# Optimization experiments

Measured on AMD Instinct MI355X. Metric: run time of the kernel, lower is better.

Reference implementation:

```python
import jax, jax.numpy as jnp
import numpy as np

N_NODES = 50000
N_EDGES = 800000
IN_DIM = 128
HID = 64
N_LAYERS = 4  # num_layers=5 in source -> 4 GINConv layers
BN_EPS = 1e-5


def setup_inputs() -> dict:
    key = jax.random.key(0)
    ks = jax.random.split(key, 16)
    h = jax.random.normal(ks[0], (N_NODES, IN_DIM), dtype=jnp.float32)
    src = jax.random.randint(ks[1], (N_EDGES,), 0, N_NODES, dtype=jnp.int32)
    dst = jax.random.randint(ks[2], (N_EDGES,), 0, N_NODES, dtype=jnp.int32)
    s = 0.05
    # layer 0 params (IN_DIM -> HID -> HID)
    W1_0 = jax.random.normal(ks[3], (IN_DIM, HID), dtype=jnp.float32) * s
    b1_0 = jnp.zeros((HID,), jnp.float32)
    W2_0 = jax.random.normal(ks[4], (HID, HID), dtype=jnp.float32) * s
    b2_0 = jnp.zeros((HID,), jnp.float32)
    g_0 = jnp.ones((HID,), jnp.float32)
    be_0 = jnp.zeros((HID,), jnp.float32)
    # layers 1..3 params stacked (HID -> HID -> HID)
    W1s = jax.random.normal(ks[5], (N_LAYERS - 1, HID, HID), dtype=jnp.float32) * s
    b1s = jnp.zeros((N_LAYERS - 1, HID), jnp.float32)
    W2s = jax.random.normal(ks[6], (N_LAYERS - 1, HID, HID), dtype=jnp.float32) * s
    b2s = jnp.zeros((N_LAYERS - 1, HID), jnp.float32)
    gs = jnp.ones((N_LAYERS - 1, HID), jnp.float32)
    bes = jnp.zeros((N_LAYERS - 1, HID), jnp.float32)
    return dict(h=h, src=src, dst=dst,
                W1_0=W1_0, b1_0=b1_0, W2_0=W2_0, b2_0=b2_0, g_0=g_0, be_0=be_0,
                W1s=W1s, b1s=b1s, W2s=W2s, b2s=b2s, gs=gs, bes=bes)


def _gin_layer(h, src, dst, W1, b1, W2, b2, gamma, beta):
    # GINConv (eps=0, sum aggregation): z = h + sum_{j->i} h_j
    agg = jax.ops.segment_sum(h[src], dst, num_segments=N_NODES)  # [N, d]
    z = h + agg
    # MLP: Linear -> ReLU -> Linear
    z = jax.nn.relu(z @ W1 + b1) @ W2 + b2
    # BatchNorm1d (training mode: batch statistics over nodes)
    mean = jnp.mean(z, axis=0)
    var = jnp.var(z, axis=0)
    z = (z - mean) * jax.lax.rsqrt(var + BN_EPS) * gamma + beta
    return jax.nn.relu(z)


def reference(h, src, dst, W1_0, b1_0, W2_0, b2_0, g_0, be_0,
              W1s, b1s, W2s, b2s, gs, bes):
    h = _gin_layer(h, src, dst, W1_0, b1_0, W2_0, b2_0, g_0, be_0)
    for i in range(N_LAYERS - 1):
        h = _gin_layer(h, src, dst, W1s[i], b1s[i], W2s[i], b2s[i], gs[i], bes[i])
    return h
```

## Files before the change

kernel.cpp:

```cpp
#include <hip/hip_runtime.h>
#include <hip/hip_bf16.h>

static constexpr int NN = 50000;
static constexpr int NE = 800000;
static constexpr float BN_EPS = 1e-5f;

static constexpr int NB  = 128;
static constexpr int NPB = 391;
static constexpr int CAP = 8192;
static constexpr int CHUNK = 2048;
static constexpr int SRNG = 12500;

static constexpr int BINABLK  = (NE + CHUNK - 1) / CHUNK;
static constexpr int PROJ0BLK = (NN + 63) / 64;

typedef short bf16x8 __attribute__((ext_vector_type(8)));
typedef float f32x4 __attribute__((ext_vector_type(4)));

__device__ __forceinline__ float bflo(unsigned u) { return __uint_as_float(u << 16); }
__device__ __forceinline__ float bfhi(unsigned u) { return __uint_as_float(u & 0xffff0000u); }
__device__ __forceinline__ unsigned short f2bf(float f) {
    unsigned u = __float_as_uint(f);
    unsigned r = (u + 0x7fffu + ((u >> 16) & 1u)) >> 16;
    return (unsigned short)r;
}

__global__ __launch_bounds__(256) void zero_kernel(int* __restrict__ ptr, int n)
{
    int i = blockIdx.x * 256 + threadIdx.x;
    if (i < n) ptr[i] = 0;
}

struct SmBinA {
    unsigned stage[CHUNK];
    int hist[NB], base[NB], gpos[NB];
};
struct SmProj0 {
    unsigned short Wt[64][136];
};

__device__ __forceinline__ void binA_body(
    SmBinA& sm, const int* __restrict__ src, const int* __restrict__ dst,
    int* __restrict__ gcount, unsigned* __restrict__ tmp, int blk)
{
    const int t = threadIdx.x;
    const int cb = blk * CHUNK;
    const int total = min(CHUNK, NE - cb);

    if (t < NB) sm.hist[t] = 0;
    __syncthreads();

    int mb[8], mslot[8];
    unsigned mv[8];
    #pragma unroll
    for (int k = 0; k < 8; ++k) {
        int e = cb + k * 256 + t;
        mb[k] = -1;
        if (e < NE) {
            int s = src[e];
            int d = dst[e];
            int b = d / NPB;
            mb[k] = b;
            mv[k] = ((unsigned)d << 16) | (unsigned)s;
            mslot[k] = atomicAdd(&sm.hist[b], 1);
        }
    }
    __syncthreads();

    if (t < NB) sm.base[t] = sm.hist[t];
    __syncthreads();
    for (int ofs = 1; ofs < NB; ofs <<= 1) {
        int v = (t >= ofs && t < NB) ? sm.base[t - ofs] : 0;
        __syncthreads();
        if (t < NB) sm.base[t] += v;
        __syncthreads();
    }
    if (t < NB && sm.hist[t] > 0)
        sm.gpos[t] = t * CAP + atomicAdd(&gcount[t], sm.hist[t]);
    __syncthreads();

    #pragma unroll
    for (int k = 0; k < 8; ++k) {
        if (mb[k] >= 0) {
            int b = mb[k];
            sm.stage[(sm.base[b] - sm.hist[b]) + mslot[k]] = mv[k];
        }
    }
    __syncthreads();

    for (int i = t; i < total; i += 256) {
        unsigned v = sm.stage[i];
        int b = (int)(v >> 16) / NPB;
        int pos = sm.gpos[b] + (i - (sm.base[b] - sm.hist[b]));
        tmp[pos] = v;
    }
}

__device__ __forceinline__ void proj0_body(
    SmProj0& sm, const float* __restrict__ hin, const float* __restrict__ W1,
    unsigned short* __restrict__ p, int blk)
{
    const int t = threadIdx.x;
    for (int i = t; i < 128 * 16; i += 256) {
        int k = i >> 4, c0 = (i & 15) * 4;
        float4 w = *reinterpret_cast<const float4*>(W1 + (size_t)k * 64 + c0);
        sm.Wt[c0 + 0][k] = f2bf(w.x); sm.Wt[c0 + 1][k] = f2bf(w.y);
        sm.Wt[c0 + 2][k] = f2bf(w.z); sm.Wt[c0 + 3][k] = f2bf(w.w);
    }
    __syncthreads();

    const int wv = t >> 6;
    const int l = t & 63;
    const int g = l >> 4;
    const int cl = l & 15;
    const int rowbase = blk * 64 + wv * 16;

    int ar = min(rowbase + cl, NN - 1);
    const float* hrow = hin + (size_t)ar * 128;
    bf16x8 a[4];
    #pragma unroll
    for (int kk = 0; kk < 4; ++kk) {
        float4 f0 = *reinterpret_cast<const float4*>(hrow + kk * 32 + 8 * g);
        float4 f1 = *reinterpret_cast<const float4*>(hrow + kk * 32 + 8 * g + 4);
        unsigned short oo[8] = { f2bf(f0.x), f2bf(f0.y), f2bf(f0.z), f2bf(f0.w),
                                 f2bf(f1.x), f2bf(f1.y), f2bf(f1.z), f2bf(f1.w) };
        a[kk] = *reinterpret_cast<bf16x8*>(oo);
    }

    f32x4 acc[4];
    #pragma unroll
    for (int ct = 0; ct < 4; ++ct) acc[ct] = (f32x4){0.f, 0.f, 0.f, 0.f};

    #pragma unroll
    for (int ct = 0; ct < 4; ++ct) {
        #pragma unroll
        for (int kk = 0; kk < 4; ++kk) {
            bf16x8 w = *reinterpret_cast<const bf16x8*>(
                &sm.Wt[ct * 16 + cl][kk * 32 + 8 * g]);
            acc[ct] = __builtin_amdgcn_mfma_f32_16x16x32_bf16(w, a[kk], acc[ct], 0, 0, 0);
        }
    }

    int gr = rowbase + cl;
    if (gr < NN) {
        #pragma unroll
        for (int ct = 0; ct < 4; ++ct) {
            unsigned lo = (unsigned)f2bf(acc[ct][0]) | ((unsigned)f2bf(acc[ct][1]) << 16);
            unsigned hi = (unsigned)f2bf(acc[ct][2]) | ((unsigned)f2bf(acc[ct][3]) << 16);
            *reinterpret_cast<uint2*>(p + (size_t)gr * 64 + ct * 16 + 4 * g) =
                make_uint2(lo, hi);
        }
    }
}

__global__ __launch_bounds__(256) void fat_kernel(
    const int* __restrict__ src, const int* __restrict__ dst,
    int* __restrict__ gcount, unsigned* __restrict__ tmp,
    const float* __restrict__ hin, const float* __restrict__ W1,
    unsigned short* __restrict__ p)
{
    __shared__ union { SmBinA a; SmProj0 w; } sm;
    if (blockIdx.x < BINABLK)
        binA_body(sm.a, src, dst, gcount, tmp, blockIdx.x);
    else
        proj0_body(sm.w, hin, W1, p, blockIdx.x - BINABLK);
}

__global__ __launch_bounds__(256) void binB_kernel(
    const unsigned* __restrict__ tmp, const int* __restrict__ gcount,
    int* __restrict__ off, int* __restrict__ eidx)
{
    __shared__ int gb[NB];
    __shared__ int hist4[NPB * 4];
    __shared__ int hs[512];
    __shared__ int cur4[NPB * 4];
    __shared__ int base_s;

    const int t = threadIdx.x;
    const int b = blockIdx.x;
    const int n0 = b * NPB;
    const int n1 = min(n0 + NPB, NN);
    const int nnodes = n1 - n0;
    const int cnt = gcount[b];

    if (t < NB) gb[t] = gcount[t];
    for (int i = t; i < NPB * 4; i += 256) hist4[i] = 0;
    __syncthreads();
    for (int ofs = 1; ofs < NB; ofs <<= 1) {
        int v = (t >= ofs && t < NB) ? gb[t - ofs] : 0;
        __syncthreads();
        if (t < NB) gb[t] += v;
        __syncthreads();
    }
    if (t == 0) base_s = (b == 0) ? 0 : gb[b - 1];
    __syncthreads();
    const int base = base_s;

    const unsigned* tb = tmp + (size_t)b * CAP;
    for (int i = t; i < cnt; i += 256) {
        unsigned v = tb[i];
        int d = (int)(v >> 16);
        int s = (int)(v & 0xffffu);
        atomicAdd(&hist4[(d - n0) * 4 + s / SRNG], 1);
    }
    __syncthreads();
    {
        int n = t;
        hs[t] = (n < NPB) ? (hist4[n * 4] + hist4[n * 4 + 1] +
                             hist4[n * 4 + 2] + hist4[n * 4 + 3]) : 0;
        n = t + 256;
        hs[t + 256] = (n < NPB) ? (hist4[n * 4] + hist4[n * 4 + 1] +
                                   hist4[n * 4 + 2] + hist4[n * 4 + 3]) : 0;
    }
    __syncthreads();
    for (int ofs = 1; ofs < 512; ofs <<= 1) {
        int a0 = (t >= ofs) ? hs[t - ofs] : 0;
        int a1 = hs[t + 256 - ofs];
        __syncthreads();
        hs[t] += a0;
        hs[t + 256] += a1;
        __syncthreads();
    }
    for (int n = t; n < nnodes; n += 256) {
        int h0 = hist4[n * 4], h1 = hist4[n * 4 + 1], h2 = hist4[n * 4 + 2];
        int tot = h0 + h1 + h2 + hist4[n * 4 + 3];
        int c = base + hs[n] - tot;
        off[n0 + n] = c;
        cur4[n * 4 + 0] = c; c += h0;
        cur4[n * 4 + 1] = c; c += h1;
        cur4[n * 4 + 2] = c; c += h2;
        cur4[n * 4 + 3] = c;
    }
    if (b == NB - 1 && t == 0) off[NN] = base + cnt;
    __syncthreads();
    for (int i = t; i < cnt; i += 256) {
        unsigned v = tb[i];
        int d = (int)(v >> 16);
        int s = (int)(v & 0xffffu);
        int pos = atomicAdd(&cur4[(d - n0) * 4 + s / SRNG], 1);
        eidx[pos] = s;
    }
}

__global__ __launch_bounds__(256) void proj_kernel(
    const unsigned short* __restrict__ zbin, const float* __restrict__ W1,
    const float* __restrict__ gsum, const float* __restrict__ gsq,
    const float* __restrict__ gamma, const float* __restrict__ beta,
    unsigned short* __restrict__ p)
{
    constexpr int RPB = 128;
    __shared__ float XsT[64][132];
    __shared__ float Ws[64][64];
    __shared__ float scs[64], shs[64];

    const int t = threadIdx.x;
    const int rowbase = blockIdx.x * RPB;

    if (t < 64) {
        const float invn = 1.f / (float)NN;
        float mean = gsum[t] * invn;
        float var  = gsq[t] * invn - mean * mean;
        float sc   = gamma[t] * rsqrtf(var + BN_EPS);
        scs[t] = sc;
        shs[t] = beta[t] - mean * sc;
    }
    __syncthreads();

    const int tc = t & 7;
    const int tr = t >> 3;
    const int c0 = tc * 8;
    const int r0 = tr * 4;

    float acc[4][8];
    #pragma unroll
    for (int i = 0; i < 4; ++i)
        #pragma unroll
        for (int j = 0; j < 8; ++j) acc[i][j] = 0.f;

    {
        const float4* wg = reinterpret_cast<const float4*>(W1);
        float4* wl = reinterpret_cast<float4*>(&Ws[0][0]);
        for (int i = t; i < 64 * 16; i += 256) wl[i] = wg[i];
    }
    {
        const uint4* hb = reinterpret_cast<const uint4*>(zbin);
        int rr = t & 31, q = t >> 5;
        for (int i = 0; i < RPB; i += 32) {
            int r = i + rr;
            int gr = rowbase + r;
            uint4 v = make_uint4(0u, 0u, 0u, 0u);
            if (gr < NN) v = hb[gr * 8 + q];
            int c = q * 8;
            float f0 = bflo(v.x), f1 = bfhi(v.x), f2 = bflo(v.y), f3 = bfhi(v.y);
            float f4 = bflo(v.z), f5 = bfhi(v.z), f6 = bflo(v.w), f7 = bfhi(v.w);
            XsT[c + 0][r] = fmaxf(f0 * scs[c + 0] + shs[c + 0], 0.f);
            XsT[c + 1][r] = fmaxf(f1 * scs[c + 1] + shs[c + 1], 0.f);
            XsT[c + 2][r] = fmaxf(f2 * scs[c + 2] + shs[c + 2], 0.f);
            XsT[c + 3][r] = fmaxf(f3 * scs[c + 3] + shs[c + 3], 0.f);
            XsT[c + 4][r] = fmaxf(f4 * scs[c + 4] + shs[c + 4], 0.f);
            XsT[c + 5][r] = fmaxf(f5 * scs[c + 5] + shs[c + 5], 0.f);
            XsT[c + 6][r] = fmaxf(f6 * scs[c + 6] + shs[c + 6], 0.f);
            XsT[c + 7][r] = fmaxf(f7 * scs[c + 7] + shs[c + 7], 0.f);
        }
    }
    __syncthreads();

    for (int k = 0; k < 64; ++k) {
        float4 xa = *reinterpret_cast<const float4*>(&XsT[k][r0]);
        float4 wa = *reinterpret_cast<const float4*>(&Ws[k][c0]);
        float4 wb = *reinterpret_cast<const float4*>(&Ws[k][c0 + 4]);
        float x[4] = { xa.x, xa.y, xa.z, xa.w };
        float w[8] = { wa.x, wa.y, wa.z, wa.w, wb.x, wb.y, wb.z, wb.w };
        #pragma unroll
        for (int i = 0; i < 4; ++i)
            #pragma unroll
            for (int j = 0; j < 8; ++j) acc[i][j] += x[i] * w[j];
    }

    #pragma unroll
    for (int i = 0; i < 4; ++i) {
        int gr = rowbase + r0 + i;
        if (gr < NN) {
            uint4 u;
            u.x = (unsigned)f2bf(acc[i][0]) | ((unsigned)f2bf(acc[i][1]) << 16);
            u.y = (unsigned)f2bf(acc[i][2]) | ((unsigned)f2bf(acc[i][3]) << 16);
            u.z = (unsigned)f2bf(acc[i][4]) | ((unsigned)f2bf(acc[i][5]) << 16);
            u.w = (unsigned)f2bf(acc[i][6]) | ((unsigned)f2bf(acc[i][7]) << 16);
            *reinterpret_cast<uint4*>(p + (size_t)gr * 64 + c0) = u;
        }
    }
}

__global__ __launch_bounds__(256) void gather_kernel(
    const unsigned short* __restrict__ p, const int* __restrict__ off,
    const int* __restrict__ eidx, const float* __restrict__ b1,
    unsigned short* __restrict__ Y)
{
    int gid = blockIdx.x * 256 + threadIdx.x;
    if (gid >= NN * 8) return;
    int row = gid >> 3;
    int q = gid & 7;

    const uint4* pb = reinterpret_cast<const uint4*>(p);
    uint4 u = pb[row * 8 + q];
    float a0 = bflo(u.x), a1 = bfhi(u.x), a2 = bflo(u.y), a3 = bfhi(u.y);
    float a4 = bflo(u.z), a5 = bfhi(u.z), a6 = bflo(u.w), a7 = bfhi(u.w);

    int e = off[row];
    const int end = off[row + 1];
    for (; e + 4 <= end; e += 4) {
        int s0 = eidx[e + 0], s1 = eidx[e + 1];
        int s2 = eidx[e + 2], s3 = eidx[e + 3];
        uint4 v0 = pb[s0 * 8 + q];
        uint4 v1 = pb[s1 * 8 + q];
        uint4 v2 = pb[s2 * 8 + q];
        uint4 v3 = pb[s3 * 8 + q];
        a0 += (bflo(v0.x) + bflo(v1.x)) + (bflo(v2.x) + bflo(v3.x));
        a1 += (bfhi(v0.x) + bfhi(v1.x)) + (bfhi(v2.x) + bfhi(v3.x));
        a2 += (bflo(v0.y) + bflo(v1.y)) + (bflo(v2.y) + bflo(v3.y));
        a3 += (bfhi(v0.y) + bfhi(v1.y)) + (bfhi(v2.y) + bfhi(v3.y));
        a4 += (bflo(v0.z) + bflo(v1.z)) + (bflo(v2.z) + bflo(v3.z));
        a5 += (bfhi(v0.z) + bfhi(v1.z)) + (bfhi(v2.z) + bfhi(v3.z));
        a6 += (bflo(v0.w) + bflo(v1.w)) + (bflo(v2.w) + bflo(v3.w));
        a7 += (bfhi(v0.w) + bfhi(v1.w)) + (bfhi(v2.w) + bfhi(v3.w));
    }
    for (; e < end; ++e) {
        uint4 v = pb[eidx[e] * 8 + q];
        a0 += bflo(v.x); a1 += bfhi(v.x); a2 += bflo(v.y); a3 += bfhi(v.y);
        a4 += bflo(v.z); a5 += bfhi(v.z); a6 += bflo(v.w); a7 += bfhi(v.w);
    }

    float4 blo = reinterpret_cast<const float4*>(b1)[q * 2];
    float4 bhi = reinterpret_cast<const float4*>(b1)[q * 2 + 1];
    a0 = fmaxf(a0 + blo.x, 0.f); a1 = fmaxf(a1 + blo.y, 0.f);
    a2 = fmaxf(a2 + blo.z, 0.f); a3 = fmaxf(a3 + blo.w, 0.f);
    a4 = fmaxf(a4 + bhi.x, 0.f); a5 = fmaxf(a5 + bhi.y, 0.f);
    a6 = fmaxf(a6 + bhi.z, 0.f); a7 = fmaxf(a7 + bhi.w, 0.f);

    uint4 o;
    o.x = (unsigned)f2bf(a0) | ((unsigned)f2bf(a1) << 16);
    o.y = (unsigned)f2bf(a2) | ((unsigned)f2bf(a3) << 16);
    o.z = (unsigned)f2bf(a4) | ((unsigned)f2bf(a5) << 16);
    o.w = (unsigned)f2bf(a6) | ((unsigned)f2bf(a7) << 16);
    reinterpret_cast<uint4*>(Y)[row * 8 + q] = o;
}

__global__ __launch_bounds__(256) void mlp2_kernel(
    const unsigned short* __restrict__ Y, const float* __restrict__ W2,
    const float* __restrict__ b2, unsigned short* __restrict__ zb,
    float* __restrict__ gsum, float* __restrict__ gsq)
{
    constexpr int RPB = 128;
    __shared__ float XsT[64][132];
    __shared__ float Ws[64][64];
    __shared__ float b2s[64], lsum[64], lsq[64];

    const int t = threadIdx.x;
    const int rowbase = blockIdx.x * RPB;

    if (t < 64) { b2s[t] = b2[t]; lsum[t] = 0.f; lsq[t] = 0.f; }

    {
        const float4* wg = reinterpret_cast<const float4*>(W2);
        float4* wl = reinterpret_cast<float4*>(&Ws[0][0]);
        for (int i = t; i < 64 * 16; i += 256) wl[i] = wg[i];
    }
    {
        const uint4* yb = reinterpret_cast<const uint4*>(Y);
        int rr = t & 31, qq = t >> 5;
        for (int i = 0; i < RPB; i += 32) {
            int r = i + rr;
            int gr = rowbase + r;
            uint4 v = make_uint4(0u, 0u, 0u, 0u);
            if (gr < NN) v = yb[gr * 8 + qq];
            int c = qq * 8;
            XsT[c + 0][r] = bflo(v.x); XsT[c + 1][r] = bfhi(v.x);
            XsT[c + 2][r] = bflo(v.y); XsT[c + 3][r] = bfhi(v.y);
            XsT[c + 4][r] = bflo(v.z); XsT[c + 5][r] = bfhi(v.z);
            XsT[c + 6][r] = bflo(v.w); XsT[c + 7][r] = bfhi(v.w);
        }
    }
    __syncthreads();

    const int tc = t & 7;
    const int tr = t >> 3;
    const int c0 = tc * 8;
    const int r0 = tr * 4;

    float acc[4][8];
    #pragma unroll
    for (int i = 0; i < 4; ++i)
        #pragma unroll
        for (int j = 0; j < 8; ++j) acc[i][j] = 0.f;

    for (int k = 0; k < 64; ++k) {
        float4 xa = *reinterpret_cast<const float4*>(&XsT[k][r0]);
        float4 wa = *reinterpret_cast<const float4*>(&Ws[k][c0]);
        float4 wb = *reinterpret_cast<const float4*>(&Ws[k][c0 + 4]);
        float x[4] = { xa.x, xa.y, xa.z, xa.w };
        float w[8] = { wa.x, wa.y, wa.z, wa.w, wb.x, wb.y, wb.z, wb.w };
        #pragma unroll
        for (int i = 0; i < 4; ++i)
            #pragma unroll
            for (int j = 0; j < 8; ++j) acc[i][j] += x[i] * w[j];
    }

    float s[8], sq[8];
    #pragma unroll
    for (int j = 0; j < 8; ++j) { s[j] = 0.f; sq[j] = 0.f; }

    #pragma unroll
    for (int i = 0; i < 4; ++i) {
        int gr = rowbase + r0 + i;
        if (gr < NN) {
            float zv[8];
            #pragma unroll
            for (int j = 0; j < 8; ++j) {
                zv[j] = acc[i][j] + b2s[c0 + j];
                s[j] += zv[j];
                sq[j] += zv[j] * zv[j];
            }
            uint4 o;
            o.x = (unsigned)f2bf(zv[0]) | ((unsigned)f2bf(zv[1]) << 16);
            o.y = (unsigned)f2bf(zv[2]) | ((unsigned)f2bf(zv[3]) << 16);
            o.z = (unsigned)f2bf(zv[4]) | ((unsigned)f2bf(zv[5]) << 16);
            o.w = (unsigned)f2bf(zv[6]) | ((unsigned)f2bf(zv[7]) << 16);
            *reinterpret_cast<uint4*>(zb + (size_t)gr * 64 + c0) = o;
        }
    }

    #pragma unroll
    for (int j = 0; j < 8; ++j) {
        s[j]  += __shfl_xor(s[j], 8);
        s[j]  += __shfl_xor(s[j], 16);
        s[j]  += __shfl_xor(s[j], 32);
        sq[j] += __shfl_xor(sq[j], 8);
        sq[j] += __shfl_xor(sq[j], 16);
        sq[j] += __shfl_xor(sq[j], 32);
    }
    if ((t & 56) == 0) {
        #pragma unroll
        for (int j = 0; j < 8; ++j) {
            atomicAdd(&lsum[c0 + j], s[j]);
            atomicAdd(&lsq[c0 + j], sq[j]);
        }
    }
    __syncthreads();
    if (t < 64) {
        atomicAdd(&gsum[t], lsum[t]);
        atomicAdd(&gsq[t], lsq[t]);
    }
}

__global__ __launch_bounds__(256) void norm_kernel(
    const unsigned short* __restrict__ zb,
    const float* __restrict__ gsum, const float* __restrict__ gsq,
    const float* __restrict__ gamma, const float* __restrict__ beta,
    float* __restrict__ out)
{
    __shared__ float sc[64], sh[64];
    int t = threadIdx.x;
    if (t < 64) {
        const float invn = 1.f / (float)NN;
        float mean = gsum[t] * invn;
        float var  = gsq[t] * invn - mean * mean;
        float s    = gamma[t] * rsqrtf(var + BN_EPS);
        sc[t] = s;
        sh[t] = beta[t] - mean * s;
    }
    __syncthreads();
    int idx = blockIdx.x * 256 + t;
    if (idx >= NN * 8) return;
    int row = idx >> 3;
    int q = idx & 7;
    int c = q * 8;
    uint4 v = reinterpret_cast<const uint4*>(zb)[idx];
    float f0 = bflo(v.x), f1 = bfhi(v.x), f2 = bflo(v.y), f3 = bfhi(v.y);
    float f4 = bflo(v.z), f5 = bfhi(v.z), f6 = bflo(v.w), f7 = bfhi(v.w);
    float4 lo, hi;
    lo.x = fmaxf(f0 * sc[c + 0] + sh[c + 0], 0.f);
    lo.y = fmaxf(f1 * sc[c + 1] + sh[c + 1], 0.f);
    lo.z = fmaxf(f2 * sc[c + 2] + sh[c + 2], 0.f);
    lo.w = fmaxf(f3 * sc[c + 3] + sh[c + 3], 0.f);
    hi.x = fmaxf(f4 * sc[c + 4] + sh[c + 4], 0.f);
    hi.y = fmaxf(f5 * sc[c + 5] + sh[c + 5], 0.f);
    hi.z = fmaxf(f6 * sc[c + 6] + sh[c + 6], 0.f);
    hi.w = fmaxf(f7 * sc[c + 7] + sh[c + 7], 0.f);
    float* o = out + (size_t)row * 64 + c;
    *reinterpret_cast<float4*>(o) = lo;
    *reinterpret_cast<float4*>(o + 4) = hi;
}

extern "C" void kernel_launch(void* const* d_in, const int* in_sizes, int n_in,
                              void* d_out, int out_size, void* d_ws, size_t ws_size,
                              hipStream_t stream)
{
    const float* h    = (const float*)d_in[0];
    const int*   src  = (const int*)d_in[1];
    const int*   dst  = (const int*)d_in[2];
    const float* W1_0 = (const float*)d_in[3];
    const float* b1_0 = (const float*)d_in[4];
    const float* W2_0 = (const float*)d_in[5];
    const float* b2_0 = (const float*)d_in[6];
    const float* g_0  = (const float*)d_in[7];
    const float* be_0 = (const float*)d_in[8];
    const float* W1st = (const float*)d_in[9];
    const float* b1st = (const float*)d_in[10];
    const float* W2st = (const float*)d_in[11];
    const float* b2st = (const float*)d_in[12];
    const float* gst  = (const float*)d_in[13];
    const float* best = (const float*)d_in[14];
    float* out = (float*)d_out;

    char* ws = (char*)d_ws;
    unsigned short* p  = (unsigned short*)ws;
    unsigned short* Y  = p + (size_t)NN * 64;
    unsigned short* zb = Y + (size_t)NN * 64;
    unsigned* tmp = (unsigned*)(zb + (size_t)NN * 64);
    int* eidx   = (int*)(tmp + (size_t)NB * CAP);
    float* stats = (float*)(eidx + NE);
    int* gcount = (int*)(stats + 512);
    int* off    = gcount + NB;

    zero_kernel<<<3, 256, 0, stream>>>((int*)stats, 512 + NB);
    fat_kernel<<<BINABLK + PROJ0BLK, 256, 0, stream>>>(
        src, dst, gcount, tmp, h, W1_0, p);
    binB_kernel<<<NB, 256, 0, stream>>>(tmp, gcount, off, eidx);

    const int gemmblk   = (NN + 127) / 128;
    const int gatherblk = (NN * 8 + 255) / 256;
    const int normblk   = (NN * 8 + 255) / 256;

    float* gs0 = stats + 0 * 128;
    gather_kernel<<<gatherblk, 256, 0, stream>>>(p, off, eidx, b1_0, Y);
    mlp2_kernel<<<gemmblk, 256, 0, stream>>>(Y, W2_0, b2_0, zb, gs0, gs0 + 64);

    const float* gammas[4] = { g_0, gst + 0, gst + 64, gst + 128 };
    const float* betas[4]  = { be_0, best + 0, best + 64, best + 128 };

    for (int l = 0; l < 3; ++l) {
        float* gsp = stats + l * 128;
        float* gsc = stats + (l + 1) * 128;
        proj_kernel<<<gemmblk, 256, 0, stream>>>(
            zb, W1st + l * 4096, gsp, gsp + 64, gammas[l], betas[l], p);
        gather_kernel<<<gatherblk, 256, 0, stream>>>(p, off, eidx, b1st + l * 64, Y);
        mlp2_kernel<<<gemmblk, 256, 0, stream>>>(
            Y, W2st + l * 4096, b2st + l * 64, zb, gsc, gsc + 64);
    }

    float* gs3 = stats + 3 * 128;
    norm_kernel<<<normblk, 256, 0, stream>>>(zb, gs3, gs3 + 64, gammas[3], betas[3], out);
}
```

Measured before the change: 232.2 us.

## Halve GEMM row tiles and refine source-range sorting of edges to eight bins

The proj and mlp2 GEMM kernels now handle 64 rows per block instead of 128, with a 4x4 per-thread tile, which doubles the block count and cuts per-thread registers and shared memory to raise occupancy. The edge binning pass now splits each destination's edges into eight source ranges instead of four, so gathers touch source rows in a more local order and cache reuse should improve. The trade-off is more blocks and more atomics in the stats reduction, and higher per-node histogram overhead during binning.

```diff
diff --git a/kernel.cpp b/kernel.cpp
--- a/kernel.cpp
+++ b/kernel.cpp
@@ -9,7 +9,8 @@
 static constexpr int NPB = 391;
 static constexpr int CAP = 8192;
 static constexpr int CHUNK = 2048;
-static constexpr int SRNG = 12500;
+static constexpr int NR   = 8;
+static constexpr int SRNG = 6250;
 
 static constexpr int BINABLK  = (NE + CHUNK - 1) / CHUNK;
 static constexpr int PROJ0BLK = (NN + 63) / 64;
@@ -171,9 +172,9 @@
     int* __restrict__ off, int* __restrict__ eidx)
 {
     __shared__ int gb[NB];
-    __shared__ int hist4[NPB * 4];
+    __shared__ int histr[NPB * NR];
     __shared__ int hs[512];
-    __shared__ int cur4[NPB * 4];
+    __shared__ int curr[NPB * NR];
     __shared__ int base_s;
 
     const int t = threadIdx.x;
@@ -184,7 +185,7 @@
     const int cnt = gcount[b];
 
     if (t < NB) gb[t] = gcount[t];
-    for (int i = t; i < NPB * 4; i += 256) hist4[i] = 0;
+    for (int i = t; i < NPB * NR; i += 256) histr[i] = 0;
     __syncthreads();
     for (int ofs = 1; ofs < NB; ofs <<= 1) {
         int v = (t >= ofs && t < NB) ? gb[t - ofs] : 0;
@@ -201,16 +202,23 @@
         unsigned v = tb[i];
         int d = (int)(v >> 16);
         int s = (int)(v & 0xffffu);
-        atomicAdd(&hist4[(d - n0) * 4 + s / SRNG], 1);
+        atomicAdd(&histr[(d - n0) * NR + s / SRNG], 1);
     }
     __syncthreads();
     {
         int n = t;
-        hs[t] = (n < NPB) ? (hist4[n * 4] + hist4[n * 4 + 1] +
-                             hist4[n * 4 + 2] + hist4[n * 4 + 3]) : 0;
-        n = t + 256;
-        hs[t + 256] = (n < NPB) ? (hist4[n * 4] + hist4[n * 4 + 1] +
-                                   hist4[n * 4 + 2] + hist4[n * 4 + 3]) : 0;
+        int tot0 = 0, tot1 = 0;
+        if (n < NPB) {
+            #pragma unroll
+            for (int r = 0; r < NR; ++r) tot0 += histr[n * NR + r];
+        }
+        int n2 = t + 256;
+        if (n2 < NPB) {
+            #pragma unroll
+            for (int r = 0; r < NR; ++r) tot1 += histr[n2 * NR + r];
+        }
+        hs[t] = tot0;
+        hs[t + 256] = tot1;
     }
     __syncthreads();
     for (int ofs = 1; ofs < 512; ofs <<= 1) {
@@ -222,14 +230,16 @@
         __syncthreads();
     }
     for (int n = t; n < nnodes; n += 256) {
-        int h0 = hist4[n * 4], h1 = hist4[n * 4 + 1], h2 = hist4[n * 4 + 2];
-        int tot = h0 + h1 + h2 + hist4[n * 4 + 3];
+        int tot = 0;
+        #pragma unroll
+        for (int r = 0; r < NR; ++r) tot += histr[n * NR + r];
         int c = base + hs[n] - tot;
         off[n0 + n] = c;
-        cur4[n * 4 + 0] = c; c += h0;
-        cur4[n * 4 + 1] = c; c += h1;
-        cur4[n * 4 + 2] = c; c += h2;
-        cur4[n * 4 + 3] = c;
+        #pragma unroll
+        for (int r = 0; r < NR; ++r) {
+            curr[n * NR + r] = c;
+            c += histr[n * NR + r];
+        }
     }
     if (b == NB - 1 && t == 0) off[NN] = base + cnt;
     __syncthreads();
@@ -237,7 +247,7 @@
         unsigned v = tb[i];
         int d = (int)(v >> 16);
         int s = (int)(v & 0xffffu);
-        int pos = atomicAdd(&cur4[(d - n0) * 4 + s / SRNG], 1);
+        int pos = atomicAdd(&curr[(d - n0) * NR + s / SRNG], 1);
         eidx[pos] = s;
     }
 }
@@ -248,8 +258,8 @@
     const float* __restrict__ gamma, const float* __restrict__ beta,
     unsigned short* __restrict__ p)
 {
-    constexpr int RPB = 128;
-    __shared__ float XsT[64][132];
+    constexpr int RPB = 64;
+    __shared__ float XsT[64][68];
     __shared__ float Ws[64][64];
     __shared__ float scs[64], shs[64];
 
@@ -265,17 +275,6 @@
         shs[t] = beta[t] - mean * sc;
     }
     __syncthreads();
-
-    const int tc = t & 7;
-    const int tr = t >> 3;
-    const int c0 = tc * 8;
-    const int r0 = tr * 4;
-
-    float acc[4][8];
-    #pragma unroll
-    for (int i = 0; i < 4; ++i)
-        #pragma unroll
-        for (int j = 0; j < 8; ++j) acc[i][j] = 0.f;
 
     {
         const float4* wg = reinterpret_cast<const float4*>(W1);
@@ -305,28 +304,35 @@
     }
     __syncthreads();
 
+    const int tc = t & 15;
+    const int tr = t >> 4;
+    const int c0 = tc * 4;
+    const int r0 = tr * 4;
+
+    float acc[4][4];
+    #pragma unroll
+    for (int i = 0; i < 4; ++i)
+        #pragma unroll
+        for (int j = 0; j < 4; ++j) acc[i][j] = 0.f;
+
     for (int k = 0; k < 64; ++k) {
         float4 xa = *reinterpret_cast<const float4*>(&XsT[k][r0]);
         float4 wa = *reinterpret_cast<const float4*>(&Ws[k][c0]);
-        float4 wb = *reinterpret_cast<const float4*>(&Ws[k][c0 + 4]);
         float x[4] = { xa.x, xa.y, xa.z, xa.w };
-        float w[8] = { wa.x, wa.y, wa.z, wa.w, wb.x, wb.y, wb.z, wb.w };
+        float w[4] = { wa.x, wa.y, wa.z, wa.w };
         #pragma unroll
         for (int i = 0; i < 4; ++i)
             #pragma unroll
-            for (int j = 0; j < 8; ++j) acc[i][j] += x[i] * w[j];
+            for (int j = 0; j < 4; ++j) acc[i][j] += x[i] * w[j];
     }
 
     #pragma unroll
     for (int i = 0; i < 4; ++i) {
         int gr = rowbase + r0 + i;
         if (gr < NN) {
-            uint4 u;
-            u.x = (unsigned)f2bf(acc[i][0]) | ((unsigned)f2bf(acc[i][1]) << 16);
-            u.y = (unsigned)f2bf(acc[i][2]) | ((unsigned)f2bf(acc[i][3]) << 16);
-            u.z = (unsigned)f2bf(acc[i][4]) | ((unsigned)f2bf(acc[i][5]) << 16);
-            u.w = (unsigned)f2bf(acc[i][6]) | ((unsigned)f2bf(acc[i][7]) << 16);
-            *reinterpret_cast<uint4*>(p + (size_t)gr * 64 + c0) = u;
+            unsigned lo = (unsigned)f2bf(acc[i][0]) | ((unsigned)f2bf(acc[i][1]) << 16);
+            unsigned hi = (unsigned)f2bf(acc[i][2]) | ((unsigned)f2bf(acc[i][3]) << 16);
+            *reinterpret_cast<uint2*>(p + (size_t)gr * 64 + c0) = make_uint2(lo, hi);
         }
     }
 }
@@ -390,8 +396,8 @@
     const float* __restrict__ b2, unsigned short* __restrict__ zb,
     float* __restrict__ gsum, float* __restrict__ gsq)
 {
-    constexpr int RPB = 128;
-    __shared__ float XsT[64][132];
+    constexpr int RPB = 64;
+    __shared__ float XsT[64][68];
     __shared__ float Ws[64][64];
     __shared__ float b2s[64], lsum[64], lsq[64];
 
@@ -422,65 +428,59 @@
     }
     __syncthreads();
 
-    const int tc = t & 7;
-    const int tr = t >> 3;
-    const int c0 = tc * 8;
+    const int tc = t & 15;
+    const int tr = t >> 4;
+    const int c0 = tc * 4;
     const int r0 = tr * 4;
 
-    float acc[4][8];
+    float acc[4][4];
     #pragma unroll
     for (int i = 0; i < 4; ++i)
         #pragma unroll
-        for (int j = 0; j < 8; ++j) acc[i][j] = 0.f;
+        for (int j = 0; j < 4; ++j) acc[i][j] = 0.f;
 
     for (int k = 0; k < 64; ++k) {
         float4 xa = *reinterpret_cast<const float4*>(&XsT[k][r0]);
         float4 wa = *reinterpret_cast<const float4*>(&Ws[k][c0]);
-        float4 wb = *reinterpret_cast<const float4*>(&Ws[k][c0 + 4]);
         float x[4] = { xa.x, xa.y, xa.z, xa.w };
-        float w[8] = { wa.x, wa.y, wa.z, wa.w, wb.x, wb.y, wb.z, wb.w };
+        float w[4] = { wa.x, wa.y, wa.z, wa.w };
         #pragma unroll
         for (int i = 0; i < 4; ++i)
             #pragma unroll
-            for (int j = 0; j < 8; ++j) acc[i][j] += x[i] * w[j];
-    }
-
-    float s[8], sq[8];
-    #pragma unroll
-    for (int j = 0; j < 8; ++j) { s[j] = 0.f; sq[j] = 0.f; }
+            for (int j = 0; j < 4; ++j) acc[i][j] += x[i] * w[j];
+    }
+
+    float s[4], sq[4];
+    #pragma unroll
+    for (int j = 0; j < 4; ++j) { s[j] = 0.f; sq[j] = 0.f; }
 
     #pragma unroll
     for (int i = 0; i < 4; ++i) {
         int gr = rowbase + r0 + i;
         if (gr < NN) {
-            float zv[8];
+            float zv[4];
             #pragma unroll
-            for (int j = 0; j < 8; ++j) {
+            for (int j = 0; j < 4; ++j) {
                 zv[j] = acc[i][j] + b2s[c0 + j];
                 s[j] += zv[j];
                 sq[j] += zv[j] * zv[j];
             }
-            uint4 o;
-            o.x = (unsigned)f2bf(zv[0]) | ((unsigned)f2bf(zv[1]) << 16);
-            o.y = (unsigned)f2bf(zv[2]) | ((unsigned)f2bf(zv[3]) << 16);
-            o.z = (unsigned)f2bf(zv[4]) | ((unsigned)f2bf(zv[5]) << 16);
-            o.w = (unsigned)f2bf(zv[6]) | ((unsigned)f2bf(zv[7]) << 16);
-            *reinterpret_cast<uint4*>(zb + (size_t)gr * 64 + c0) = o;
-        }
-    }
-
-    #pragma unroll
-    for (int j = 0; j < 8; ++j) {
-        s[j]  += __shfl_xor(s[j], 8);
+            unsigned lo = (unsigned)f2bf(zv[0]) | ((unsigned)f2bf(zv[1]) << 16);
+            unsigned hi = (unsigned)f2bf(zv[2]) | ((unsigned)f2bf(zv[3]) << 16);
+            *reinterpret_cast<uint2*>(zb + (size_t)gr * 64 + c0) = make_uint2(lo, hi);
+        }
+    }
+
+    #pragma unroll
+    for (int j = 0; j < 4; ++j) {
         s[j]  += __shfl_xor(s[j], 16);
         s[j]  += __shfl_xor(s[j], 32);
-        sq[j] += __shfl_xor(sq[j], 8);
         sq[j] += __shfl_xor(sq[j], 16);
         sq[j] += __shfl_xor(sq[j], 32);
     }
-    if ((t & 56) == 0) {
-        #pragma unroll
-        for (int j = 0; j < 8; ++j) {
+    if ((t & 48) == 0) {
+        #pragma unroll
+        for (int j = 0; j < 4; ++j) {
             atomicAdd(&lsum[c0 + j], s[j]);
             atomicAdd(&lsq[c0 + j], sq[j]);
         }
@@ -567,7 +567,7 @@
         src, dst, gcount, tmp, h, W1_0, p);
     binB_kernel<<<NB, 256, 0, stream>>>(tmp, gcount, off, eidx);
 
-    const int gemmblk   = (NN + 127) / 128;
+    const int gemmblk   = (NN + 63) / 64;
     const int gatherblk = (NN * 8 + 255) / 256;
     const int normblk   = (NN * 8 + 255) / 256;
 
```

After: 258.0 us. +11.1%, slower.
